# Performance work log

Hardware: AMD Instinct MI355X
Metric: run time of the kernel (lower is better)

## Reference

```python
import jax, jax.numpy as jnp
import numpy as np
import math

EPS_LN = 1e-5
SCALE = 16.0  # cosine_sim_scale


def layer_norm(x, g):
    mean = jnp.mean(x, axis=-1, keepdims=True)
    var = jnp.var(x, axis=-1, keepdims=True)  # biased, matches unbiased=False
    return (x - mean) * jax.lax.rsqrt(var + EPS_LN) * g


def l2norm(t):
    n = jnp.linalg.norm(t, axis=-1, keepdims=True)
    return t / jnp.maximum(n, 1e-12)


def setup_inputs() -> dict:
    key = jax.random.key(0)
    ks = jax.random.split(key, 4)
    b, n, dim, h, dh = 4, 2048, 1024, 8, 64
    inner = h * dh
    x = jax.random.normal(ks[0], (b, n, dim), dtype=jnp.float32)
    Wq = jax.random.normal(ks[1], (dim, inner), dtype=jnp.float32) * (dim ** -0.5)
    Wkv = jax.random.normal(ks[2], (dim, 2 * dh), dtype=jnp.float32) * (dim ** -0.5)
    Wout = jax.random.normal(ks[3], (inner, dim), dtype=jnp.float32) * (inner ** -0.5)
    norm_g = jnp.ones((dim,), dtype=jnp.float32)
    out_norm_g = jnp.ones((dim,), dtype=jnp.float32)
    return {"x": x, "norm_g": norm_g, "Wq": Wq, "Wkv": Wkv, "Wout": Wout,
            "out_norm_g": out_norm_g}


def reference(x, norm_g, Wq, Wkv, Wout, out_norm_g):
    b, n, dim = x.shape
    h = 8
    dh = Wkv.shape[-1] // 2
    xn = layer_norm(x, norm_g)
    q = xn @ Wq                      # [b, n, h*dh]
    kv = xn @ Wkv                    # [b, n, 2*dh]
    k, v = kv[..., :dh], kv[..., dh:]
    q = q.reshape(b, n, h, dh).transpose(0, 2, 1, 3)  # [b, h, n, dh]
    q = q * SCALE                    # cancelled by l2norm, kept for fidelity
    q = l2norm(q)
    k = l2norm(k)
    rs = math.sqrt(SCALE)
    q = q * rs
    k = k * rs
    sim = jnp.einsum('bhid,bjd->bhij', q, k)          # [b, h, n, n]
    attn = jax.nn.softmax(sim.astype(jnp.float32), axis=-1).astype(sim.dtype)
    out = jnp.einsum('bhij,bjd->bhid', attn, v)       # [b, h, n, dh]
    out = out.transpose(0, 2, 1, 3).reshape(b, n, h * dh)
    out = out @ Wout
    return layer_norm(out, out_norm_g)
```

## Files before the change

### kernel.cpp

```cpp
#include <hip/hip_runtime.h>
#include <hip/hip_bf16.h>

typedef __attribute__((ext_vector_type(8))) short short8;
typedef __attribute__((ext_vector_type(4))) float floatx4;
typedef __attribute__((ext_vector_type(16))) float floatx16;

__device__ __forceinline__ float bf2f(ushort u) {
    return __uint_as_float(((unsigned int)u) << 16);
}
__device__ __forceinline__ ushort f2bf(float f) {
    unsigned int u = __float_as_uint(f);
    unsigned int r = (u + 0x7FFFu + ((u >> 16) & 1u)) >> 16;
    return (ushort)r;
}
__device__ __forceinline__ unsigned int pk2(float a, float b) {
    union { __hip_bfloat162 h; unsigned int u; } cv;
    cv.h = __float22bfloat162_rn(make_float2(a, b));
    return cv.u;
}
__device__ __forceinline__ float scrub(float v, float lim) {
    return fminf(fmaxf(v, -lim), lim);
}
__device__ __forceinline__ void glds16(const ushort* g, ushort* l) {
    __builtin_amdgcn_global_load_lds((const __attribute__((address_space(1))) void*)g,
                                     (__attribute__((address_space(3))) void*)l, 16, 0, 0);
}

__device__ __forceinline__ bool detect_bf16(const ushort* __restrict__ probe) {
    const int lane = threadIdx.x & 63;
    ushort u = probe[(lane & 31) * 2];
    int e = (u >> 7) & 0xFF;
    bool pl = (e >= 117) && (e <= 131) && (lane < 32);
    return __popcll(__ballot(pl)) >= 16;
}

__device__ __forceinline__ void do_transpose(const void* __restrict__ in,
                                             ushort* __restrict__ out,
                                             int bx, int by, int in_rs, int out_rs,
                                             bool ib, ushort* tile ) {
    const int tx = threadIdx.x & 31, ty = threadIdx.x >> 5;
    #pragma unroll
    for (int rr = 0; rr < 32; rr += 8) {
        size_t idx = (size_t)(by * 32 + ty + rr) * in_rs + bx * 32 + tx;
        float v = ib ? bf2f(((const ushort*)in)[idx]) : ((const float*)in)[idx];
        tile[(ty + rr) * 33 + tx] = f2bf(scrub(v, 1e8f));
    }
    __syncthreads();
    #pragma unroll
    for (int rr = 0; rr < 32; rr += 8) {
        int r = bx * 32 + ty + rr;
        int c = by * 32 + tx;
        out[(size_t)r * out_rs + c] = tile[tx * 33 + (ty + rr)];
    }
}

__global__ __launch_bounds__(256) void prep_kernel(const void* __restrict__ xin,
                                                   const void* __restrict__ gin,
                                                   const void* __restrict__ Wq,
                                                   const void* __restrict__ Wkv,
                                                   ushort* __restrict__ xn,
                                                   ushort* __restrict__ wcatT,
                                                   const ushort* __restrict__ probe) {
    const bool ib = detect_bf16(probe);
    const int id = blockIdx.x;
    __shared__ ushort tile[32 * 33];
    __shared__ float red[8];

    if (id >= 8192) {
        if (id < 8704) {
            int t = id - 8192;
            do_transpose(Wq, wcatT, t & 15, t >> 4, 512, 1024, ib, tile);
        } else {
            int t = id - 8704;
            do_transpose(Wkv, wcatT + (size_t)512 * 1024, t & 3, t >> 2, 128, 1024, ib, tile);
        }
        return;
    }

    const int row = id;
    const int tid = threadIdx.x;
    float v0, v1, v2, v3, g0, g1, g2, g3;
    if (ib) {
        uint2 u = *(const uint2*)((const ushort*)xin + (size_t)row * 1024 + tid * 4);
        v0 = bf2f((ushort)(u.x & 0xFFFF)); v1 = bf2f((ushort)(u.x >> 16));
        v2 = bf2f((ushort)(u.y & 0xFFFF)); v3 = bf2f((ushort)(u.y >> 16));
        uint2 gu = *(const uint2*)((const ushort*)gin + tid * 4);
        g0 = bf2f((ushort)(gu.x & 0xFFFF)); g1 = bf2f((ushort)(gu.x >> 16));
        g2 = bf2f((ushort)(gu.y & 0xFFFF)); g3 = bf2f((ushort)(gu.y >> 16));
    } else {
        float4 xv = *(const float4*)((const float*)xin + (size_t)row * 1024 + tid * 4);
        v0 = xv.x; v1 = xv.y; v2 = xv.z; v3 = xv.w;
        float4 gv = *(const float4*)((const float*)gin + tid * 4);
        g0 = gv.x; g1 = gv.y; g2 = gv.z; g3 = gv.w;
    }
    v0 = scrub(v0, 1e8f); v1 = scrub(v1, 1e8f); v2 = scrub(v2, 1e8f); v3 = scrub(v3, 1e8f);
    g0 = scrub(g0, 1e8f); g1 = scrub(g1, 1e8f); g2 = scrub(g2, 1e8f); g3 = scrub(g3, 1e8f);

    float s  = v0 + v1 + v2 + v3;
    float sq = v0 * v0 + v1 * v1 + v2 * v2 + v3 * v3;
    #pragma unroll
    for (int off = 1; off < 64; off <<= 1) {
        s  += __shfl_xor(s, off);
        sq += __shfl_xor(sq, off);
    }
    const int w = tid >> 6, lane = tid & 63;
    if (lane == 0) { red[w] = s; red[w + 4] = sq; }
    __syncthreads();
    float S  = red[0] + red[1] + red[2] + red[3];
    float SQ = red[4] + red[5] + red[6] + red[7];

    float mean = S * (1.0f / 1024.0f);
    float var  = SQ * (1.0f / 1024.0f) - mean * mean;
    float rstd = rsqrtf(fmaxf(var, 0.0f) + 1e-5f);

    uint2 ov;
    ov.x = pk2((v0 - mean) * rstd * g0, (v1 - mean) * rstd * g1);
    ov.y = pk2((v2 - mean) * rstd * g2, (v3 - mean) * rstd * g3);
    *(uint2*)(xn + (size_t)row * 1024 + tid * 4) = ov;
}

__global__ __launch_bounds__(256) void wout_tr_kernel(const void* __restrict__ Wout,
                                                      ushort* __restrict__ woT,
                                                      const ushort* __restrict__ probe) {
    const bool ib = detect_bf16(probe);
    __shared__ ushort tile[32 * 33];
    do_transpose(Wout, woT, blockIdx.x, blockIdx.y, 1024, 512, ib, tile);
}

__global__ __launch_bounds__(256) void ln2_kernel(const ushort* __restrict__ y,
                                                  const void* __restrict__ gin,
                                                  void* __restrict__ out,
                                                  const ushort* __restrict__ probe) {
    const bool ob = detect_bf16(probe);
    const int row = blockIdx.x;
    const int tid = threadIdx.x;

    uint2 u = *(const uint2*)(y + (size_t)row * 1024 + tid * 4);
    float v0 = scrub(bf2f((ushort)(u.x & 0xFFFF)), 1e8f);
    float v1 = scrub(bf2f((ushort)(u.x >> 16)),    1e8f);
    float v2 = scrub(bf2f((ushort)(u.y & 0xFFFF)), 1e8f);
    float v3 = scrub(bf2f((ushort)(u.y >> 16)),    1e8f);

    float g0, g1, g2, g3;
    if (ob) {
        uint2 gu = *(const uint2*)((const ushort*)gin + tid * 4);
        g0 = bf2f((ushort)(gu.x & 0xFFFF)); g1 = bf2f((ushort)(gu.x >> 16));
        g2 = bf2f((ushort)(gu.y & 0xFFFF)); g3 = bf2f((ushort)(gu.y >> 16));
    } else {
        float4 gv = *(const float4*)((const float*)gin + tid * 4);
        g0 = gv.x; g1 = gv.y; g2 = gv.z; g3 = gv.w;
    }
    g0 = scrub(g0, 1e8f); g1 = scrub(g1, 1e8f); g2 = scrub(g2, 1e8f); g3 = scrub(g3, 1e8f);

    float s  = v0 + v1 + v2 + v3;
    float sq = v0 * v0 + v1 * v1 + v2 * v2 + v3 * v3;
    #pragma unroll
    for (int off = 1; off < 64; off <<= 1) {
        s  += __shfl_xor(s, off);
        sq += __shfl_xor(sq, off);
    }
    __shared__ float red[8];
    const int w = tid >> 6, lane = tid & 63;
    if (lane == 0) { red[w] = s; red[w + 4] = sq; }
    __syncthreads();
    float S  = red[0] + red[1] + red[2] + red[3];
    float SQ = red[4] + red[5] + red[6] + red[7];

    float mean = S * (1.0f / 1024.0f);
    float var  = SQ * (1.0f / 1024.0f) - mean * mean;
    float rstd = rsqrtf(fmaxf(var, 0.0f) + 1e-5f);

    float o0 = (v0 - mean) * rstd * g0;
    float o1 = (v1 - mean) * rstd * g1;
    float o2 = (v2 - mean) * rstd * g2;
    float o3 = (v3 - mean) * rstd * g3;
    if (ob) {
        uint2 ov;
        ov.x = pk2(o0, o1);
        ov.y = pk2(o2, o3);
        *(uint2*)((ushort*)out + (size_t)row * 1024 + tid * 4) = ov;
    } else {
        *(float4*)((float*)out + (size_t)row * 1024 + tid * 4) = make_float4(o0, o1, o2, o3);
    }
}

__global__ __launch_bounds__(256) void gemm_qkv(const ushort* __restrict__ A,
                                                const ushort* __restrict__ Bt,
                                                ushort* __restrict__ qb,
                                                ushort* __restrict__ kb,
                                                ushort* __restrict__ vt) {
    __shared__ ushort a_t[64 * 32];
    __shared__ ushort b_t[64 * 32];

    const int bx = blockIdx.x;
    const int n0 = bx * 64, m0 = blockIdx.y * 64;
    const int tid = threadIdx.x;
    const int w = tid >> 6, lane = tid & 63;
    const int fm = lane & 15, quad = lane >> 4;
    const int K = 1024;

    const ushort* ag = A + (size_t)(m0 + (tid >> 2)) * K + (tid & 3) * 8;
    const ushort* bg = Bt + (size_t)(n0 + (tid >> 2)) * K + (tid & 3) * 8;
    ushort* la = a_t + w * 512;
    ushort* lb = b_t + w * 512;

    floatx4 acc[4];
    floatx4 zero4 = {0.0f, 0.0f, 0.0f, 0.0f};
    #pragma unroll
    for (int nt = 0; nt < 4; nt++) acc[nt] = zero4;

    union U8 { uint4 u4; short8 s8; };

    for (int k0 = 0; k0 < K; k0 += 32) {
        __syncthreads();
        glds16(ag + k0, la);
        glds16(bg + k0, lb);
        __syncthreads();

        U8 af;
        af.u4 = *(const uint4*)&a_t[(w * 16 + fm) * 32 + quad * 8];
        #pragma unroll
        for (int nt = 0; nt < 4; nt++) {
            U8 bf;
            bf.u4 = *(const uint4*)&b_t[(nt * 16 + fm) * 32 + quad * 8];
            acc[nt] = __builtin_amdgcn_mfma_f32_16x16x32_bf16(af.s8, bf.s8, acc[nt], 0, 0, 0);
        }
    }

    if (bx < 9) {
        const float qsc = (bx < 8) ? 5.7707801636f : 4.0f;
        float sc[4];
        #pragma unroll
        for (int r = 0; r < 4; r++) {
            float ss = acc[0][r] * acc[0][r] + acc[1][r] * acc[1][r]
                     + acc[2][r] * acc[2][r] + acc[3][r] * acc[3][r];
            ss += __shfl_xor(ss, 1);
            ss += __shfl_xor(ss, 2);
            ss += __shfl_xor(ss, 4);
            ss += __shfl_xor(ss, 8);
            sc[r] = qsc / fmaxf(sqrtf(ss), 1e-12f);
        }
        if (bx < 8) {
            ushort* op = qb + n0;
            #pragma unroll
            for (int nt = 0; nt < 4; nt++)
                #pragma unroll
                for (int r = 0; r < 4; r++)
                    op[(size_t)(m0 + w * 16 + quad * 4 + r) * 512 + nt * 16 + fm] =
                        f2bf(acc[nt][r] * sc[r]);
        } else {
            const int bb = m0 >> 11;
            const int kblk = ((m0 & 2047) >> 5) + (w >> 1);
            const int qsw = ((quad & 1) << 1) | (quad >> 1);
            ushort* op = kb + (size_t)bb * 131072 + kblk * 2048
                       + (w & 1) * 128 + qsw * 32 + (fm & 7);
            #pragma unroll
            for (int nt = 0; nt < 4; nt++) {
                const int oct = nt * 2 + (fm >> 3);
                #pragma unroll
                for (int r = 0; r < 4; r++)
                    op[oct * 256 + r * 8] = f2bf(acc[nt][r] * sc[r]);
            }
        }
    } else {
        const int bb = m0 >> 11;
        const int kblk = ((m0 & 2047) >> 5) + (w >> 1);
        const int koct = ((w & 1) * 2 + (quad >> 1)) & 3;
        ushort* vb = vt + (size_t)bb * 131072 + kblk * 2048 + koct * 512 + (quad & 1) * 4;
        #pragma unroll
        for (int nt = 0; nt < 4; nt++) {
            uint2 pv;
            pv.x = pk2(acc[nt][0], acc[nt][1]);
            pv.y = pk2(acc[nt][2], acc[nt][3]);
            *(uint2*)(vb + (nt * 16 + fm) * 8) = pv;
        }
    }
}

__global__ __launch_bounds__(256) void gemm_bt128(const ushort* __restrict__ A,
                                                  const ushort* __restrict__ Bt,
                                                  ushort* __restrict__ C,
                                                  int M, int N, int K) {
    __shared__ ushort a_t[128][32];
    __shared__ ushort b_t[128][32];

    const int n0 = blockIdx.x * 128, m0 = blockIdx.y * 128;
    const int tid = threadIdx.x;
    const int w = tid >> 6, lane = tid & 63;
    const int fm = lane & 15, quad = lane >> 4;

    const int c0 = tid, c1 = tid + 256;
    const ushort* ag0 = A + (size_t)(m0 + (c0 >> 2)) * K + (c0 & 3) * 8;
    const ushort* ag1 = A + (size_t)(m0 + (c1 >> 2)) * K + (c1 & 3) * 8;
    const ushort* bg0 = Bt + (size_t)(n0 + (c0 >> 2)) * K + (c0 & 3) * 8;
    const ushort* bg1 = Bt + (size_t)(n0 + (c1 >> 2)) * K + (c1 & 3) * 8;
    ushort* la0 = &a_t[0][0] + w * 512;
    ushort* la1 = &a_t[0][0] + 2048 + w * 512;
    ushort* lb0 = &b_t[0][0] + w * 512;
    ushort* lb1 = &b_t[0][0] + 2048 + w * 512;

    floatx4 acc[2][8];
    floatx4 zero4 = {0.0f, 0.0f, 0.0f, 0.0f};
    #pragma unroll
    for (int mt = 0; mt < 2; mt++)
        #pragma unroll
        for (int nt = 0; nt < 8; nt++) acc[mt][nt] = zero4;

    union U8 { uint4 u4; short8 s8; };

    for (int k0 = 0; k0 < K; k0 += 32) {
        __syncthreads();
        glds16(ag0 + k0, la0);
        glds16(ag1 + k0, la1);
        glds16(bg0 + k0, lb0);
        glds16(bg1 + k0, lb1);
        __syncthreads();

        U8 af[2];
        #pragma unroll
        for (int mt = 0; mt < 2; mt++)
            af[mt].u4 = *(const uint4*)&a_t[w * 32 + mt * 16 + fm][quad * 8];
        #pragma unroll
        for (int nt = 0; nt < 8; nt++) {
            U8 bf;
            bf.u4 = *(const uint4*)&b_t[nt * 16 + fm][quad * 8];
            acc[0][nt] = __builtin_amdgcn_mfma_f32_16x16x32_bf16(af[0].s8, bf.s8, acc[0][nt], 0, 0, 0);
            acc[1][nt] = __builtin_amdgcn_mfma_f32_16x16x32_bf16(af[1].s8, bf.s8, acc[1][nt], 0, 0, 0);
        }
    }

    #pragma unroll
    for (int mt = 0; mt < 2; mt++)
        #pragma unroll
        for (int nt = 0; nt < 8; nt++)
            #pragma unroll
            for (int r = 0; r < 4; r++)
                C[(size_t)(m0 + w * 32 + mt * 16 + quad * 4 + r) * N + n0 + nt * 16 + fm] =
                    f2bf(acc[mt][nt][r]);
}

__global__ __launch_bounds__(512, 4) void attn_kernel(const ushort* __restrict__ q,
                                                      const ushort* __restrict__ kb,
                                                      const ushort* __restrict__ vt,
                                                      ushort* __restrict__ out) {
    __shared__ ushort smem[17408];
    ushort* k_t = smem;
    ushort* v_t = smem + 8192;

    const int i0 = blockIdx.x * 128;
    const int h0 = blockIdx.y, b = blockIdx.z;
    const int tid = threadIdx.x, w = tid >> 6, lane = tid & 63;
    const int qg = w & 3;
    const int ks = w >> 2;
    const int cq = lane & 31;
    const int hi = lane >> 5;

    union U8 { uint4 u4; short8 s8; };

    const ushort* qbase = q + (size_t)(b * 2048 + i0 + qg * 32 + cq) * 512 + h0 * 64 + hi * 8;
    U8 qf[4];
    #pragma unroll
    for (int dm = 0; dm < 4; dm++) qf[dm].u4 = *(const uint4*)(qbase + dm * 16);

    floatx16 acc0, acc1;
    #pragma unroll
    for (int i = 0; i < 16; i++) { acc0[i] = 0.0f; acc1[i] = 0.0f; }
    float lsum = 0.0f;

    const ushort* kSrc = kb + (size_t)b * 131072 + ks * 65536 + lane * 8;
    const ushort* vSrc = vt + (size_t)b * 131072 + ks * 65536 + lane * 8;

    ushort* kT = k_t + ks * 4096;
    ushort* vT = v_t + ks * 4096;

    auto stageK = [&](int s, int buf) {
        glds16(kSrc + s * 2048 + qg * 512, kT + buf * 2048 + qg * 512);
    };
    auto stageV = [&](int s, int buf) {
        glds16(vSrc + s * 2048 + qg * 512, vT + buf * 2048 + qg * 512);
    };

    auto qk_exp = [&](int buf, U8& pb0, U8& pb1) {
        const int bo = buf * 2048;
        floatx16 st;
        #pragma unroll
        for (int i = 0; i < 16; i++) st[i] = -23.0831206f;
        #pragma unroll
        for (int dm = 0; dm < 4; dm++) {
            U8 kf;
            kf.u4 = *(const uint4*)&kT[bo + (2 * dm + hi) * 256 + cq * 8];
            st = __builtin_amdgcn_mfma_f32_32x32x16_bf16(kf.s8, qf[dm].s8, st, 0, 0, 0);
        }
        float p_[16];
        #pragma unroll
        for (int r = 0; r < 16; r++) p_[r] = __builtin_amdgcn_exp2f(st[r]);
        lsum += (((p_[0] + p_[1]) + (p_[2] + p_[3])) + ((p_[4] + p_[5]) + (p_[6] + p_[7])))
              + (((p_[8] + p_[9]) + (p_[10] + p_[11])) + ((p_[12] + p_[13]) + (p_[14] + p_[15])));
        pb0.u4.x = pk2(p_[0], p_[1]);   pb0.u4.y = pk2(p_[2], p_[3]);
        pb0.u4.z = pk2(p_[4], p_[5]);   pb0.u4.w = pk2(p_[6], p_[7]);
        pb1.u4.x = pk2(p_[8], p_[9]);   pb1.u4.y = pk2(p_[10], p_[11]);
        pb1.u4.z = pk2(p_[12], p_[13]); pb1.u4.w = pk2(p_[14], p_[15]);
    };

    auto pv = [&](int buf, U8 pb0, U8 pb1) {
        const int bo = buf * 2048;
        U8 vf;
        vf.u4 = *(const uint4*)&vT[bo + (0 + hi) * 512 + cq * 8];
        acc0 = __builtin_amdgcn_mfma_f32_32x32x16_bf16(vf.s8, pb0.s8, acc0, 0, 0, 0);
        vf.u4 = *(const uint4*)&vT[bo + (2 + hi) * 512 + cq * 8];
        acc0 = __builtin_amdgcn_mfma_f32_32x32x16_bf16(vf.s8, pb1.s8, acc0, 0, 0, 0);
        vf.u4 = *(const uint4*)&vT[bo + (0 + hi) * 512 + (32 + cq) * 8];
        acc1 = __builtin_amdgcn_mfma_f32_32x32x16_bf16(vf.s8, pb0.s8, acc1, 0, 0, 0);
        vf.u4 = *(const uint4*)&vT[bo + (2 + hi) * 512 + (32 + cq) * 8];
        acc1 = __builtin_amdgcn_mfma_f32_32x32x16_bf16(vf.s8, pb1.s8, acc1, 0, 0, 0);
    };

    U8 pA0, pA1, pB0, pB1;

    stageK(0, 0);
    __syncthreads();

    stageK(1, 1);
    stageV(0, 0);
    qk_exp(0, pA0, pA1);
    __syncthreads();

    for (int s = 1; s < 32; s += 2) {
        if (s + 1 < 32) stageK(s + 1, 0);
        stageV(s, 1);
        qk_exp(1, pB0, pB1);
        pv(0, pA0, pA1);
        __syncthreads();

        if (s + 1 < 32) {
            if (s + 2 < 32) stageK(s + 2, 1);
            stageV(s + 1, 0);
            qk_exp(0, pA0, pA1);
            pv(1, pB0, pB1);
            __syncthreads();
        }
    }
    pv(1, pB0, pB1);
    __syncthreads();

    float* row = (float*)smem + (qg * 64 + lane) * 34;
    if (ks == 1) {
        #pragma unroll
        for (int i = 0; i < 16; i++) { row[i] = acc0[i]; row[16 + i] = acc1[i]; }
        row[32] = lsum;
    }
    __syncthreads();
    if (ks == 1) return;
    #pragma unroll
    for (int i = 0; i < 16; i++) { acc0[i] += row[i]; acc1[i] += row[16 + i]; }
    lsum += row[32];
    lsum += __shfl_xor(lsum, 32);
    float li = 1.0f / fmaxf(lsum, 1e-30f);

    ushort* ob = out + (size_t)(b * 2048 + i0 + qg * 32 + cq) * 512 + h0 * 64 + hi * 4;
    #pragma unroll
    for (int t = 0; t < 4; t++) {
        uint2 ov;
        ov.x = pk2(acc0[4 * t] * li, acc0[4 * t + 1] * li);
        ov.y = pk2(acc0[4 * t + 2] * li, acc0[4 * t + 3] * li);
        *(uint2*)(ob + t * 8) = ov;
        ov.x = pk2(acc1[4 * t] * li, acc1[4 * t + 1] * li);
        ov.y = pk2(acc1[4 * t + 2] * li, acc1[4 * t + 3] * li);
        *(uint2*)(ob + 32 + t * 8) = ov;
    }
}

extern "C" void kernel_launch(void* const* d_in, const int* in_sizes, int n_in,
                              void* d_out, int out_size, void* d_ws, size_t ws_size,
                              hipStream_t stream) {
    const void* x          = d_in[0];
    const void* norm_g     = d_in[1];
    const void* Wq         = d_in[2];
    const void* Wkv        = d_in[3];
    const void* Wout       = d_in[4];
    const void* out_norm_g = d_in[5];
    const ushort* probe = (const ushort*)d_in[0];
    ushort* ws = (ushort*)d_ws;

    const size_t M1 = 1024 * 1024 / 2;
    ushort* xn    = (ushort*)d_out;
    ushort* ao    = (ushort*)d_out;
    ushort* woT   = (ushort*)((char*)d_out + (8u << 20));
    ushort* qb    = ws;
    ushort* kb    = ws + 8 * M1;
    ushort* vt    = ws + 9 * M1;
    ushort* wcatT = ws + 11 * M1;
    ushort* y     = ws;

    prep_kernel<<<8832, 256, 0, stream>>>(x, norm_g, Wq, Wkv, xn, wcatT, probe);

    gemm_qkv<<<dim3(10, 128), 256, 0, stream>>>(xn, wcatT, qb, kb, vt);

    wout_tr_kernel<<<dim3(32, 16), 256, 0, stream>>>(Wout, woT, probe);

    attn_kernel<<<dim3(16, 8, 4), 512, 0, stream>>>(qb, kb, vt, ao);

    gemm_bt128<<<dim3(8, 64), 256, 0, stream>>>(ao, woT, y, 8192, 1024, 512);

    ln2_kernel<<<8192, 256, 0, stream>>>(y, out_norm_g, d_out, probe);
}
```

Before: 206.2 us.

## Enlarge QKV projection GEMM tiles to 128x128 with fused K/V epilogue

The QKV projection GEMM moves from 64x64 tiles to 128x128 tiles, giving each wave a 32x128 sub-tile with two A fragments reused across eight B fragments. The K and V columns now land in the same block, so one epilogue does the l2norm scaling for K and the transposed V store, and each Q block normalizes two heads. This cuts LDS and global reloads per MFMA, but the grid shrinks from 1280 to 320 blocks, which may underfill the GPU's compute units and raises register use.

After: 203.5 us. Within noise of the previous version (-1.3%).

```diff
diff --git a/kernel.cpp b/kernel.cpp
--- a/kernel.cpp
+++ b/kernel.cpp
@@ -184,95 +184,121 @@
     }
 }
 
-__global__ __launch_bounds__(256) void gemm_qkv(const ushort* __restrict__ A,
-                                                const ushort* __restrict__ Bt,
-                                                ushort* __restrict__ qb,
-                                                ushort* __restrict__ kb,
-                                                ushort* __restrict__ vt) {
-    __shared__ ushort a_t[64 * 32];
-    __shared__ ushort b_t[64 * 32];
+__global__ __launch_bounds__(256) void gemm_qkv128(const ushort* __restrict__ A,
+                                                   const ushort* __restrict__ Bt,
+                                                   ushort* __restrict__ qb,
+                                                   ushort* __restrict__ kb,
+                                                   ushort* __restrict__ vt) {
+    __shared__ ushort a_t[128][32];
+    __shared__ ushort b_t[128][32];
 
     const int bx = blockIdx.x;
-    const int n0 = bx * 64, m0 = blockIdx.y * 64;
+    const int n0 = bx * 128, m0 = blockIdx.y * 128;
     const int tid = threadIdx.x;
     const int w = tid >> 6, lane = tid & 63;
     const int fm = lane & 15, quad = lane >> 4;
     const int K = 1024;
 
-    const ushort* ag = A + (size_t)(m0 + (tid >> 2)) * K + (tid & 3) * 8;
-    const ushort* bg = Bt + (size_t)(n0 + (tid >> 2)) * K + (tid & 3) * 8;
-    ushort* la = a_t + w * 512;
-    ushort* lb = b_t + w * 512;
-
-    floatx4 acc[4];
+    const int c0 = tid, c1 = tid + 256;
+    const ushort* ag0 = A + (size_t)(m0 + (c0 >> 2)) * K + (c0 & 3) * 8;
+    const ushort* ag1 = A + (size_t)(m0 + (c1 >> 2)) * K + (c1 & 3) * 8;
+    const ushort* bg0 = Bt + (size_t)(n0 + (c0 >> 2)) * K + (c0 & 3) * 8;
+    const ushort* bg1 = Bt + (size_t)(n0 + (c1 >> 2)) * K + (c1 & 3) * 8;
+    ushort* la0 = &a_t[0][0] + w * 512;
+    ushort* la1 = &a_t[0][0] + 2048 + w * 512;
+    ushort* lb0 = &b_t[0][0] + w * 512;
+    ushort* lb1 = &b_t[0][0] + 2048 + w * 512;
+
+    floatx4 acc[2][8];
     floatx4 zero4 = {0.0f, 0.0f, 0.0f, 0.0f};
     #pragma unroll
-    for (int nt = 0; nt < 4; nt++) acc[nt] = zero4;
+    for (int mt = 0; mt < 2; mt++)
+        #pragma unroll
+        for (int nt = 0; nt < 8; nt++) acc[mt][nt] = zero4;
 
     union U8 { uint4 u4; short8 s8; };
 
     for (int k0 = 0; k0 < K; k0 += 32) {
         __syncthreads();
-        glds16(ag + k0, la);
-        glds16(bg + k0, lb);
+        glds16(ag0 + k0, la0);
+        glds16(ag1 + k0, la1);
+        glds16(bg0 + k0, lb0);
+        glds16(bg1 + k0, lb1);
         __syncthreads();
 
-        U8 af;
-        af.u4 = *(const uint4*)&a_t[(w * 16 + fm) * 32 + quad * 8];
-        #pragma unroll
-        for (int nt = 0; nt < 4; nt++) {
+        U8 af[2];
+        #pragma unroll
+        for (int mt = 0; mt < 2; mt++)
+            af[mt].u4 = *(const uint4*)&a_t[w * 32 + mt * 16 + fm][quad * 8];
+        #pragma unroll
+        for (int nt = 0; nt < 8; nt++) {
             U8 bf;
-            bf.u4 = *(const uint4*)&b_t[(nt * 16 + fm) * 32 + quad * 8];
-            acc[nt] = __builtin_amdgcn_mfma_f32_16x16x32_bf16(af.s8, bf.s8, acc[nt], 0, 0, 0);
-        }
-    }
-
-    if (bx < 9) {
-        const float qsc = (bx < 8) ? 5.7707801636f : 4.0f;
-        float sc[4];
-        #pragma unroll
-        for (int r = 0; r < 4; r++) {
-            float ss = acc[0][r] * acc[0][r] + acc[1][r] * acc[1][r]
-                     + acc[2][r] * acc[2][r] + acc[3][r] * acc[3][r];
-            ss += __shfl_xor(ss, 1);
-            ss += __shfl_xor(ss, 2);
-            ss += __shfl_xor(ss, 4);
-            ss += __shfl_xor(ss, 8);
-            sc[r] = qsc / fmaxf(sqrtf(ss), 1e-12f);
-        }
-        if (bx < 8) {
-            ushort* op = qb + n0;
+            bf.u4 = *(const uint4*)&b_t[nt * 16 + fm][quad * 8];
+            acc[0][nt] = __builtin_amdgcn_mfma_f32_16x16x32_bf16(af[0].s8, bf.s8, acc[0][nt], 0, 0, 0);
+            acc[1][nt] = __builtin_amdgcn_mfma_f32_16x16x32_bf16(af[1].s8, bf.s8, acc[1][nt], 0, 0, 0);
+        }
+    }
+
+    if (bx < 4) {
+        const float qsc = 5.7707801636f;
+        #pragma unroll
+        for (int mt = 0; mt < 2; mt++) {
+            float scA[4], scB[4];
             #pragma unroll
-            for (int nt = 0; nt < 4; nt++)
+            for (int r = 0; r < 4; r++) {
+                float sa = acc[mt][0][r] * acc[mt][0][r] + acc[mt][1][r] * acc[mt][1][r]
+                         + acc[mt][2][r] * acc[mt][2][r] + acc[mt][3][r] * acc[mt][3][r];
+                float sb = acc[mt][4][r] * acc[mt][4][r] + acc[mt][5][r] * acc[mt][5][r]
+                         + acc[mt][6][r] * acc[mt][6][r] + acc[mt][7][r] * acc[mt][7][r];
+                sa += __shfl_xor(sa, 1); sb += __shfl_xor(sb, 1);
+                sa += __shfl_xor(sa, 2); sb += __shfl_xor(sb, 2);
+                sa += __shfl_xor(sa, 4); sb += __shfl_xor(sb, 4);
+                sa += __shfl_xor(sa, 8); sb += __shfl_xor(sb, 8);
+                scA[r] = qsc / fmaxf(sqrtf(sa), 1e-12f);
+                scB[r] = qsc / fmaxf(sqrtf(sb), 1e-12f);
+            }
+            #pragma unroll
+            for (int nt = 0; nt < 8; nt++)
                 #pragma unroll
                 for (int r = 0; r < 4; r++)
-                    op[(size_t)(m0 + w * 16 + quad * 4 + r) * 512 + nt * 16 + fm] =
-                        f2bf(acc[nt][r] * sc[r]);
-        } else {
-            const int bb = m0 >> 11;
-            const int kblk = ((m0 & 2047) >> 5) + (w >> 1);
-            const int qsw = ((quad & 1) << 1) | (quad >> 1);
-            ushort* op = kb + (size_t)bb * 131072 + kblk * 2048
-                       + (w & 1) * 128 + qsw * 32 + (fm & 7);
+                    qb[(size_t)(m0 + w * 32 + mt * 16 + quad * 4 + r) * 512 + n0 + nt * 16 + fm] =
+                        f2bf(acc[mt][nt][r] * ((nt < 4) ? scA[r] : scB[r]));
+        }
+    } else {
+        const int bb = m0 >> 11;
+        const int kblk = ((m0 & 2047) >> 5) + w;
+        const int qsw = ((quad & 1) << 1) | (quad >> 1);
+        #pragma unroll
+        for (int mt = 0; mt < 2; mt++) {
+            float sck[4];
+            #pragma unroll
+            for (int r = 0; r < 4; r++) {
+                float ss = acc[mt][0][r] * acc[mt][0][r] + acc[mt][1][r] * acc[mt][1][r]
+                         + acc[mt][2][r] * acc[mt][2][r] + acc[mt][3][r] * acc[mt][3][r];
+                ss += __shfl_xor(ss, 1);
+                ss += __shfl_xor(ss, 2);
+                ss += __shfl_xor(ss, 4);
+                ss += __shfl_xor(ss, 8);
+                sck[r] = 4.0f / fmaxf(sqrtf(ss), 1e-12f);
+            }
+            ushort* kop = kb + (size_t)bb * 131072 + kblk * 2048
+                        + mt * 128 + qsw * 32 + (fm & 7);
             #pragma unroll
             for (int nt = 0; nt < 4; nt++) {
                 const int oct = nt * 2 + (fm >> 3);
                 #pragma unroll
                 for (int r = 0; r < 4; r++)
-                    op[oct * 256 + r * 8] = f2bf(acc[nt][r] * sc[r]);
+                    kop[oct * 256 + r * 8] = f2bf(acc[mt][nt][r] * sck[r]);
             }
-        }
-    } else {
-        const int bb = m0 >> 11;
-        const int kblk = ((m0 & 2047) >> 5) + (w >> 1);
-        const int koct = ((w & 1) * 2 + (quad >> 1)) & 3;
-        ushort* vb = vt + (size_t)bb * 131072 + kblk * 2048 + koct * 512 + (quad & 1) * 4;
-        #pragma unroll
-        for (int nt = 0; nt < 4; nt++) {
-            uint2 pv;
-            pv.x = pk2(acc[nt][0], acc[nt][1]);
-            pv.y = pk2(acc[nt][2], acc[nt][3]);
-            *(uint2*)(vb + (nt * 16 + fm) * 8) = pv;
+            const int koct = mt * 2 + (quad >> 1);
+            ushort* vb = vt + (size_t)bb * 131072 + kblk * 2048 + koct * 512 + (quad & 1) * 4;
+            #pragma unroll
+            for (int nt = 4; nt < 8; nt++) {
+                uint2 pv;
+                pv.x = pk2(acc[mt][nt][0], acc[mt][nt][1]);
+                pv.y = pk2(acc[mt][nt][2], acc[mt][nt][3]);
+                *(uint2*)(vb + ((nt - 4) * 16 + fm) * 8) = pv;
+            }
         }
     }
 }
@@ -494,7 +520,7 @@
 
     prep_kernel<<<8832, 256, 0, stream>>>(x, norm_g, Wq, Wkv, xn, wcatT, probe);
 
-    gemm_qkv<<<dim3(10, 128), 256, 0, stream>>>(xn, wcatT, qb, kb, vt);
+    gemm_qkv128<<<dim3(5, 64), 256, 0, stream>>>(xn, wcatT, qb, kb, vt);
 
     wout_tr_kernel<<<dim3(32, 16), 256, 0, stream>>>(Wout, woT, probe);
 
```
